# Kernel optimization log

Measured on AMD Instinct MI355X. Metric: run time of the kernel, lower is better.

Reference implementation:

```python
import jax, jax.numpy as jnp
import numpy as np

EPS = 1e-5


def setup_inputs() -> dict:
    key = jax.random.key(0)
    ks = jax.random.split(key, 8)
    g, p, d, h, w = 32, 64, 512, 24, 8
    hw = h * w
    return {
        "gal_fea": jax.random.normal(ks[0], (g, d, h, w), dtype=jnp.float32),
        "prob_fea": jax.random.normal(ks[1], (p, d, h, w), dtype=jnp.float32),
        "bn_weight": jnp.ones((1,), jnp.float32),
        "bn_bias": jnp.zeros((1,), jnp.float32),
        "bn_mean": jax.random.normal(ks[2], (1,), jnp.float32) * 0.1,
        "bn_var": jax.random.uniform(ks[3], (1,), jnp.float32, 0.5, 1.5),
        "fc_weight": jax.random.normal(ks[4], (1, 2 * hw), jnp.float32) * 0.05,
        "fc_bias": jnp.zeros((1,), jnp.float32),
        "lbn_weight": jnp.ones((1,), jnp.float32),
        "lbn_bias": jnp.zeros((1,), jnp.float32),
        "lbn_mean": jax.random.normal(ks[5], (1,), jnp.float32) * 0.1,
        "lbn_var": jax.random.uniform(ks[6], (1,), jnp.float32, 0.5, 1.5),
    }


def reference(gal_fea, prob_fea, bn_weight, bn_bias, bn_mean, bn_var,
              fc_weight, fc_bias, lbn_weight, lbn_bias, lbn_mean, lbn_var):
    g, d, h, w = gal_fea.shape
    p = prob_fea.shape[0]
    hw = h * w
    # 1x1 conv with probe pixels as kernels == batched correlation (QK^T style)
    gal = gal_fea.reshape(g, d, hw)                                  # [g, d, hw_x]
    ker = jnp.transpose(prob_fea, (0, 2, 3, 1)).reshape(p, hw, d)    # [p, hw_y, d]
    s = jnp.einsum('gdx,pyd->gpyx', gal, ker)                        # [g, p, hw_y, hw_x]
    # dual-axis max pooling, then concat: [g, p, 2*hw]
    score = jnp.concatenate([s.max(axis=2), s.max(axis=3)], axis=-1)
    # BatchNorm1d(1) in eval mode: scalar affine with running stats
    score = (score - bn_mean) * (bn_weight / jnp.sqrt(bn_var + EPS)) + bn_bias
    # fc: Linear(2*hw, 1)
    score = score.reshape(g * p, 2 * hw) @ fc_weight[0] + fc_bias[0]  # [g*p]
    score = score.reshape(g, p)
    # logit BatchNorm1d(1), eval mode
    score = (score - lbn_mean) * (lbn_weight / jnp.sqrt(lbn_var + EPS)) + lbn_bias
    return jax.nn.sigmoid(score / 10.0)
```

## Files before the change

### kernel.cpp

```cpp
#include <hip/hip_runtime.h>
#include <hip/hip_bf16.h>
#include <cstdint>
#include <cstddef>

#define NG 32
#define NP 64
#define ND 512
#define HW 192
#define KT2 16
#define EPSV 1e-5f

typedef _Float16 half8 __attribute__((ext_vector_type(8)));
typedef float floatx4 __attribute__((ext_vector_type(4)));
typedef float floatx16 __attribute__((ext_vector_type(16)));

__global__ __launch_bounds__(256) void prep_tiles(const float* __restrict__ gal,
                                                  const float* __restrict__ prob,
                                                  _Float16* __restrict__ galT3,
                                                  _Float16* __restrict__ probT3) {
  const int z = blockIdx.x;
  const int kt2 = blockIdx.y;
  const float* src;
  _Float16* dst;
  if (z < NP) {
    src = prob + (size_t)z * ND * HW;
    dst = probT3 + (size_t)z * KT2 * 6144;
  } else {
    src = gal + (size_t)(z - NP) * ND * HW;
    dst = galT3 + (size_t)(z - NP) * KT2 * 6144;
  }
  src += (size_t)kt2 * 32 * HW;
  dst += (size_t)kt2 * 6144;
  const int t = threadIdx.x;
#pragma unroll
  for (int r = 0; r < 3; ++r) {
    const int h = r * 256 + t;
    const int rb = h >> 7, kc = (h >> 6) & 1, hi = (h >> 5) & 1, l31 = h & 31;
    const float* sp = src + (size_t)(kc * 16 + hi * 8) * HW + rb * 32 + l31;
    half8 v;
#pragma unroll
    for (int j = 0; j < 8; ++j) v[j] = (_Float16)sp[(size_t)j * HW];
    *(half8*)(dst + (size_t)h * 8) = v;
  }
}

__device__ __forceinline__ void g2l16(const void* g, void* l) {
  __builtin_amdgcn_global_load_lds(
      (const __attribute__((address_space(1))) void*)g,
      (__attribute__((address_space(3))) void*)l, 16, 0, 0);
}

__global__ __launch_bounds__(256, 2) void qaconv_main(
    const _Float16* __restrict__ galT3, const _Float16* __restrict__ probT3,
    const float* __restrict__ bn_w, const float* __restrict__ bn_b,
    const float* __restrict__ bn_m, const float* __restrict__ bn_v,
    const float* __restrict__ fc_w, const float* __restrict__ fc_b,
    const float* __restrict__ lbn_w, const float* __restrict__ lbn_b,
    const float* __restrict__ lbn_m, const float* __restrict__ lbn_v,
    float* __restrict__ out) {
  __shared__ __align__(16) char shmem[50688];
  __shared__ float colp[2][HW];
  __shared__ float wsum[4];
  char* bufs = shmem;
  float(*rowbuf)[66] = (float(*)[66])shmem;

  const int bid = blockIdx.x;
  const int g = bid >> 6, p = bid & 63;

  const int t = threadIdx.x;
  const int lane = t & 63, wid = t >> 6;
  const int wr = wid & 1;
  const int wc = wid >> 1;
  const int l31 = lane & 31, hi = lane >> 5;

  const _Float16* pAl = probT3 + (size_t)p * KT2 * 6144 + wid * 512 + lane * 8;
  const _Float16* pBl = galT3 + (size_t)g * KT2 * 6144 + wid * 512 + lane * 8;
  const int sdst = wid * 1024;

  floatx16 acc[3][3];
#pragma unroll
  for (int ii = 0; ii < 3; ++ii)
#pragma unroll
    for (int jj = 0; jj < 3; ++jj) acc[ii][jj] = (floatx16)0.f;

#define STAGE(kt_, b_)                                               \
  {                                                                  \
    char* db_ = bufs + (b_)*24576 + sdst;                            \
    const _Float16* sa_ = pAl + (size_t)(kt_)*6144;                  \
    const _Float16* sb_ = pBl + (size_t)(kt_)*6144;                  \
    _Pragma("unroll") for (int r_ = 0; r_ < 3; ++r_)                 \
        g2l16(sa_ + (size_t)r_ * 2048, db_ + r_ * 4096);             \
    _Pragma("unroll") for (int r_ = 0; r_ < 3; ++r_)                 \
        g2l16(sb_ + (size_t)r_ * 2048, db_ + 12288 + r_ * 4096);     \
  }

#define KC_BODY(kc_)                                                             \
  {                                                                              \
    half8 af[3], bf[3];                                                          \
    const int off_ = (kc_)*1024 + hi * 512 + l31 * 16;                           \
    af[0] = *(const half8*)(bA + (wr * 3 + 0) * 2048 + off_);                    \
    af[1] = *(const half8*)(bA + (wr * 3 + 1) * 2048 + off_);                    \
    af[2] = *(const half8*)(bA + (wr * 3 + 2) * 2048 + off_);                    \
    bf[0] = *(const half8*)(bB + (wc * 3 + 0) * 2048 + off_);                    \
    bf[1] = *(const half8*)(bB + (wc * 3 + 1) * 2048 + off_);                    \
    bf[2] = *(const half8*)(bB + (wc * 3 + 2) * 2048 + off_);                    \
    __builtin_amdgcn_s_setprio(1);                                               \
    _Pragma("unroll") for (int ii = 0; ii < 3; ++ii)                             \
        _Pragma("unroll") for (int jj = 0; jj < 3; ++jj)                         \
            acc[ii][jj] = __builtin_amdgcn_mfma_f32_32x32x16_f16(af[ii], bf[jj], \
                                                                 acc[ii][jj], 0, 0, 0); \
    __builtin_amdgcn_s_setprio(0);                                               \
  }

  STAGE(0, 0);
  __syncthreads();

  for (int kt = 0; kt < KT2; ++kt) {
    if (kt < KT2 - 1) STAGE(kt + 1, (kt & 1) ^ 1);
    const char* bA = bufs + (kt & 1) * 24576;
    const char* bB = bA + 12288;
    KC_BODY(0)
    KC_BODY(1)
    __syncthreads();
  }

#pragma unroll
  for (int fb = 0; fb < 3; ++fb) {
    float v = -3.4e38f;
#pragma unroll
    for (int fa = 0; fa < 3; ++fa)
#pragma unroll
      for (int e = 0; e < 16; ++e) v = fmaxf(v, acc[fa][fb][e]);
    v = fmaxf(v, __shfl_xor(v, 32));
    if (lane < 32) colp[wr][wc * 96 + fb * 32 + lane] = v;
  }
#pragma unroll
  for (int fa = 0; fa < 3; ++fa)
#pragma unroll
    for (int e = 0; e < 16; ++e) {
      float rv = acc[fa][0][e];
      rv = fmaxf(rv, acc[fa][1][e]);
      rv = fmaxf(rv, acc[fa][2][e]);
      const int Y = wr * 96 + fa * 32 + (e & 3) + 8 * (e >> 2) + 4 * hi;
      rowbuf[Y][wc * 32 + l31] = rv;
    }
  __syncthreads();

  float partial = 0.f;
  if (t < HW) {
    const float* rb = rowbuf[t];
    float rmax = -3.4e38f;
#pragma unroll
    for (int j = 0; j < 16; ++j) {
      const floatx4 v = *(const floatx4*)&rb[j * 4];
      rmax = fmaxf(rmax, fmaxf(fmaxf(v[0], v[1]), fmaxf(v[2], v[3])));
    }
    const float cmax = fmaxf(colp[0][t], colp[1][t]);
    const float scale = bn_w[0] / sqrtf(bn_v[0] + EPSV);
    const float bm = bn_m[0], bb = bn_b[0];
    partial = ((cmax - bm) * scale + bb) * fc_w[t] +
              ((rmax - bm) * scale + bb) * fc_w[HW + t];
  }
#pragma unroll
  for (int off = 1; off < 64; off <<= 1) partial += __shfl_xor(partial, off);
  if (lane == 0) wsum[wid] = partial;
  __syncthreads();
  if (t == 0) {
    const float sum = fc_b[0] + wsum[0] + wsum[1] + wsum[2] + wsum[3];
    const float logit = (sum - lbn_m[0]) * (lbn_w[0] / sqrtf(lbn_v[0] + EPSV)) + lbn_b[0];
    out[bid] = 1.f / (1.f + expf(-logit * 0.1f));
  }
#undef STAGE
#undef KC_BODY
}

__global__ __launch_bounds__(256) void qaconv_naive(
    const float* __restrict__ gal, const float* __restrict__ prob,
    const float* __restrict__ bn_w, const float* __restrict__ bn_b,
    const float* __restrict__ bn_m, const float* __restrict__ bn_v,
    const float* __restrict__ fc_w, const float* __restrict__ fc_b,
    const float* __restrict__ lbn_w, const float* __restrict__ lbn_b,
    const float* __restrict__ lbn_m, const float* __restrict__ lbn_v,
    float* __restrict__ out) {
  __shared__ float prow[ND];
  __shared__ float rowmaxs[HW];
  __shared__ float colmaxs[HW];
  __shared__ float red[4];
  const int bid = blockIdx.x;
  const int g = bid >> 6, p = bid & 63;
  const int t = threadIdx.x, lane = t & 63, wid = t >> 6;
  const float* gp = gal + (size_t)g * ND * HW;
  const float* pp = prob + (size_t)p * ND * HW;
  float colmax = -3.4e38f;
  for (int y = 0; y < HW; ++y) {
    for (int k = t; k < ND; k += 256) prow[k] = pp[(size_t)k * HW + y];
    __syncthreads();
    float sv = -3.4e38f;
    if (t < HW) {
      sv = 0.f;
      for (int k = 0; k < ND; ++k) sv = fmaf(prow[k], gp[(size_t)k * HW + t], sv);
      colmax = fmaxf(colmax, sv);
    }
    float m = sv;
#pragma unroll
    for (int off = 1; off < 64; off <<= 1) m = fmaxf(m, __shfl_xor(m, off));
    if (lane == 0) red[wid] = m;
    __syncthreads();
    if (t == 0) rowmaxs[y] = fmaxf(fmaxf(red[0], red[1]), fmaxf(red[2], red[3]));
    __syncthreads();
  }
  if (t < HW) colmaxs[t] = colmax;
  __syncthreads();
  float partial = 0.f;
  for (int j = t; j < 2 * HW; j += 256) {
    const float v = (j < HW) ? colmaxs[j] : rowmaxs[j - HW];
    const float sc = (v - bn_m[0]) * (bn_w[0] / sqrtf(bn_v[0] + EPSV)) + bn_b[0];
    partial += sc * fc_w[j];
  }
#pragma unroll
  for (int off = 1; off < 64; off <<= 1) partial += __shfl_xor(partial, off);
  if (lane == 0) red[wid] = partial;
  __syncthreads();
  if (t == 0) {
    const float sum = fc_b[0] + red[0] + red[1] + red[2] + red[3];
    const float logit = (sum - lbn_m[0]) * (lbn_w[0] / sqrtf(lbn_v[0] + EPSV)) + lbn_b[0];
    out[bid] = 1.f / (1.f + expf(-logit * 0.1f));
  }
}

extern "C" void kernel_launch(void* const* d_in, const int* in_sizes, int n_in,
                              void* d_out, int out_size, void* d_ws, size_t ws_size,
                              hipStream_t stream) {
  const float* gal = (const float*)d_in[0];
  const float* prob = (const float*)d_in[1];
  const float* bn_w = (const float*)d_in[2];
  const float* bn_b = (const float*)d_in[3];
  const float* bn_m = (const float*)d_in[4];
  const float* bn_v = (const float*)d_in[5];
  const float* fc_w = (const float*)d_in[6];
  const float* fc_b = (const float*)d_in[7];
  const float* lbn_w = (const float*)d_in[8];
  const float* lbn_b = (const float*)d_in[9];
  const float* lbn_m = (const float*)d_in[10];
  const float* lbn_v = (const float*)d_in[11];
  float* out = (float*)d_out;

  const size_t probT3_elems = (size_t)NP * KT2 * 6144;
  const size_t galT3_elems = (size_t)NG * KT2 * 6144;
  const size_t ws_needed = (probT3_elems + galT3_elems) * sizeof(_Float16);
  if (ws_size >= ws_needed) {
    _Float16* probT3 = (_Float16*)d_ws;
    _Float16* galT3 = probT3 + probT3_elems;
    prep_tiles<<<dim3(NP + NG, KT2), dim3(256), 0, stream>>>(gal, prob, galT3, probT3);
    qaconv_main<<<dim3(NG * NP), dim3(256), 0, stream>>>(
        galT3, probT3, bn_w, bn_b, bn_m, bn_v, fc_w, fc_b, lbn_w, lbn_b, lbn_m, lbn_v, out);
  } else {
    qaconv_naive<<<dim3(NG * NP), dim3(256), 0, stream>>>(
        gal, prob, bn_w, bn_b, bn_m, bn_v, fc_w, fc_b, lbn_w, lbn_b, lbn_m, lbn_v, out);
  }
}
```

Before: 91.38 us.

## Load MFMA fragments directly from global memory, dropping LDS staging

The prep kernel now writes fp16 data in per-lane MFMA fragment order, with 16-deep k-slices staged through LDS so the reads from the source are coalesced. The main kernel loads its A/B fragments straight from global memory into registers, double-buffered in registers, and drops the LDS ping-pong buffers and the per-k-step barriers. The row-max reduction now uses cross-lane shuffles instead of a large LDS row buffer. This removes LDS traffic and synchronisation and frees shared memory. The cost is that every wave re-reads its fragments from global memory or L2, with more register pressure and less reuse across the waves in a block.

```diff
diff --git a/kernel.cpp b/kernel.cpp
--- a/kernel.cpp
+++ b/kernel.cpp
@@ -7,62 +7,59 @@
 #define NP 64
 #define ND 512
 #define HW 192
-#define KT2 16
+#define KS 32
 #define EPSV 1e-5f
 
 typedef _Float16 half8 __attribute__((ext_vector_type(8)));
 typedef float floatx4 __attribute__((ext_vector_type(4)));
 typedef float floatx16 __attribute__((ext_vector_type(16)));
 
-__global__ __launch_bounds__(256) void prep_tiles(const float* __restrict__ gal,
-                                                  const float* __restrict__ prob,
-                                                  _Float16* __restrict__ galT3,
-                                                  _Float16* __restrict__ probT3) {
+__global__ __launch_bounds__(256) void prep_frag(const float* __restrict__ gal,
+                                                 const float* __restrict__ prob,
+                                                 _Float16* __restrict__ galT4,
+                                                 _Float16* __restrict__ probT4) {
+  __shared__ float lds[16 * 192];
   const int z = blockIdx.x;
-  const int kt2 = blockIdx.y;
+  const int ks = blockIdx.y;
   const float* src;
   _Float16* dst;
   if (z < NP) {
     src = prob + (size_t)z * ND * HW;
-    dst = probT3 + (size_t)z * KT2 * 6144;
+    dst = probT4 + (size_t)z * 98304;
   } else {
     src = gal + (size_t)(z - NP) * ND * HW;
-    dst = galT3 + (size_t)(z - NP) * KT2 * 6144;
-  }
-  src += (size_t)kt2 * 32 * HW;
-  dst += (size_t)kt2 * 6144;
+    dst = galT4 + (size_t)(z - NP) * 98304;
+  }
+  src += (size_t)ks * 16 * HW;
+  dst += (size_t)ks * 3072;
   const int t = threadIdx.x;
 #pragma unroll
-  for (int r = 0; r < 3; ++r) {
+  for (int i = 0; i < 12; ++i) lds[i * 256 + t] = src[i * 256 + t];
+  __syncthreads();
+#pragma unroll
+  for (int r = 0; r < 2; ++r) {
     const int h = r * 256 + t;
-    const int rb = h >> 7, kc = (h >> 6) & 1, hi = (h >> 5) & 1, l31 = h & 31;
-    const float* sp = src + (size_t)(kc * 16 + hi * 8) * HW + rb * 32 + l31;
-    half8 v;
-#pragma unroll
-    for (int j = 0; j < 8; ++j) v[j] = (_Float16)sp[(size_t)j * HW];
-    *(half8*)(dst + (size_t)h * 8) = v;
-  }
-}
-
-__device__ __forceinline__ void g2l16(const void* g, void* l) {
-  __builtin_amdgcn_global_load_lds(
-      (const __attribute__((address_space(1))) void*)g,
-      (__attribute__((address_space(3))) void*)l, 16, 0, 0);
+    if (h < 384) {
+      const int rb = h >> 6, hi = (h >> 5) & 1, l31 = h & 31;
+      half8 v;
+#pragma unroll
+      for (int j = 0; j < 8; ++j) v[j] = (_Float16)lds[(hi * 8 + j) * 192 + rb * 32 + l31];
+      *(half8*)(dst + (size_t)h * 8) = v;
+    }
+  }
 }
 
 __global__ __launch_bounds__(256, 2) void qaconv_main(
-    const _Float16* __restrict__ galT3, const _Float16* __restrict__ probT3,
+    const _Float16* __restrict__ galT4, const _Float16* __restrict__ probT4,
     const float* __restrict__ bn_w, const float* __restrict__ bn_b,
     const float* __restrict__ bn_m, const float* __restrict__ bn_v,
     const float* __restrict__ fc_w, const float* __restrict__ fc_b,
     const float* __restrict__ lbn_w, const float* __restrict__ lbn_b,
     const float* __restrict__ lbn_m, const float* __restrict__ lbn_v,
     float* __restrict__ out) {
-  __shared__ __align__(16) char shmem[50688];
   __shared__ float colp[2][HW];
+  __shared__ float rowpart[2][HW];
   __shared__ float wsum[4];
-  char* bufs = shmem;
-  float(*rowbuf)[66] = (float(*)[66])shmem;
 
   const int bid = blockIdx.x;
   const int g = bid >> 6, p = bid & 63;
@@ -73,9 +70,8 @@
   const int wc = wid >> 1;
   const int l31 = lane & 31, hi = lane >> 5;
 
-  const _Float16* pAl = probT3 + (size_t)p * KT2 * 6144 + wid * 512 + lane * 8;
-  const _Float16* pBl = galT3 + (size_t)g * KT2 * 6144 + wid * 512 + lane * 8;
-  const int sdst = wid * 1024;
+  const _Float16* pA = probT4 + (size_t)p * 98304 + wr * 1536 + lane * 8;
+  const _Float16* pB = galT4 + (size_t)g * 98304 + wc * 1536 + lane * 8;
 
   floatx16 acc[3][3];
 #pragma unroll
@@ -83,45 +79,38 @@
 #pragma unroll
     for (int jj = 0; jj < 3; ++jj) acc[ii][jj] = (floatx16)0.f;
 
-#define STAGE(kt_, b_)                                               \
-  {                                                                  \
-    char* db_ = bufs + (b_)*24576 + sdst;                            \
-    const _Float16* sa_ = pAl + (size_t)(kt_)*6144;                  \
-    const _Float16* sb_ = pBl + (size_t)(kt_)*6144;                  \
-    _Pragma("unroll") for (int r_ = 0; r_ < 3; ++r_)                 \
-        g2l16(sa_ + (size_t)r_ * 2048, db_ + r_ * 4096);             \
-    _Pragma("unroll") for (int r_ = 0; r_ < 3; ++r_)                 \
-        g2l16(sb_ + (size_t)r_ * 2048, db_ + 12288 + r_ * 4096);     \
-  }
-
-#define KC_BODY(kc_)                                                             \
+#define LOADF(AF, BF, ks_)                                   \
+  {                                                          \
+    const _Float16* a_ = pA + (size_t)(ks_)*3072;            \
+    const _Float16* b_ = pB + (size_t)(ks_)*3072;            \
+    AF[0] = *(const half8*)(a_);                             \
+    AF[1] = *(const half8*)(a_ + 512);                       \
+    AF[2] = *(const half8*)(a_ + 1024);                      \
+    BF[0] = *(const half8*)(b_);                             \
+    BF[1] = *(const half8*)(b_ + 512);                       \
+    BF[2] = *(const half8*)(b_ + 1024);                      \
+  }
+
+#define MFMAS(AF, BF)                                                            \
   {                                                                              \
-    half8 af[3], bf[3];                                                          \
-    const int off_ = (kc_)*1024 + hi * 512 + l31 * 16;                           \
-    af[0] = *(const half8*)(bA + (wr * 3 + 0) * 2048 + off_);                    \
-    af[1] = *(const half8*)(bA + (wr * 3 + 1) * 2048 + off_);                    \
-    af[2] = *(const half8*)(bA + (wr * 3 + 2) * 2048 + off_);                    \
-    bf[0] = *(const half8*)(bB + (wc * 3 + 0) * 2048 + off_);                    \
-    bf[1] = *(const half8*)(bB + (wc * 3 + 1) * 2048 + off_);                    \
-    bf[2] = *(const half8*)(bB + (wc * 3 + 2) * 2048 + off_);                    \
     __builtin_amdgcn_s_setprio(1);                                               \
     _Pragma("unroll") for (int ii = 0; ii < 3; ++ii)                             \
         _Pragma("unroll") for (int jj = 0; jj < 3; ++jj)                         \
-            acc[ii][jj] = __builtin_amdgcn_mfma_f32_32x32x16_f16(af[ii], bf[jj], \
+            acc[ii][jj] = __builtin_amdgcn_mfma_f32_32x32x16_f16(AF[ii], BF[jj], \
                                                                  acc[ii][jj], 0, 0, 0); \
     __builtin_amdgcn_s_setprio(0);                                               \
   }
 
-  STAGE(0, 0);
-  __syncthreads();
-
-  for (int kt = 0; kt < KT2; ++kt) {
-    if (kt < KT2 - 1) STAGE(kt + 1, (kt & 1) ^ 1);
-    const char* bA = bufs + (kt & 1) * 24576;
-    const char* bB = bA + 12288;
-    KC_BODY(0)
-    KC_BODY(1)
-    __syncthreads();
+  half8 af0[3], bf0[3], af1[3], bf1[3];
+  LOADF(af0, bf0, 0)
+  LOADF(af1, bf1, 1)
+  for (int ks = 0; ks < KS; ks += 2) {
+    const int n0 = (ks + 2 < KS) ? ks + 2 : 30;
+    const int n1 = (ks + 3 < KS) ? ks + 3 : 31;
+    MFMAS(af0, bf0)
+    LOADF(af0, bf0, n0)
+    MFMAS(af1, bf1)
+    LOADF(af1, bf1, n1)
   }
 
 #pragma unroll
@@ -138,23 +127,22 @@
   for (int fa = 0; fa < 3; ++fa)
 #pragma unroll
     for (int e = 0; e < 16; ++e) {
-      float rv = acc[fa][0][e];
-      rv = fmaxf(rv, acc[fa][1][e]);
-      rv = fmaxf(rv, acc[fa][2][e]);
-      const int Y = wr * 96 + fa * 32 + (e & 3) + 8 * (e >> 2) + 4 * hi;
-      rowbuf[Y][wc * 32 + l31] = rv;
+      float rv = fmaxf(fmaxf(acc[fa][0][e], acc[fa][1][e]), acc[fa][2][e]);
+      rv = fmaxf(rv, __shfl_xor(rv, 1));
+      rv = fmaxf(rv, __shfl_xor(rv, 2));
+      rv = fmaxf(rv, __shfl_xor(rv, 4));
+      rv = fmaxf(rv, __shfl_xor(rv, 8));
+      rv = fmaxf(rv, __shfl_xor(rv, 16));
+      if (l31 == 0) {
+        const int Y = wr * 96 + fa * 32 + (e & 3) + 8 * (e >> 2) + 4 * hi;
+        rowpart[wc][Y] = rv;
+      }
     }
   __syncthreads();
 
   float partial = 0.f;
   if (t < HW) {
-    const float* rb = rowbuf[t];
-    float rmax = -3.4e38f;
-#pragma unroll
-    for (int j = 0; j < 16; ++j) {
-      const floatx4 v = *(const floatx4*)&rb[j * 4];
-      rmax = fmaxf(rmax, fmaxf(fmaxf(v[0], v[1]), fmaxf(v[2], v[3])));
-    }
+    const float rmax = fmaxf(rowpart[0][t], rowpart[1][t]);
     const float cmax = fmaxf(colp[0][t], colp[1][t]);
     const float scale = bn_w[0] / sqrtf(bn_v[0] + EPSV);
     const float bm = bn_m[0], bb = bn_b[0];
@@ -170,8 +158,8 @@
     const float logit = (sum - lbn_m[0]) * (lbn_w[0] / sqrtf(lbn_v[0] + EPSV)) + lbn_b[0];
     out[bid] = 1.f / (1.f + expf(-logit * 0.1f));
   }
-#undef STAGE
-#undef KC_BODY
+#undef LOADF
+#undef MFMAS
 }
 
 __global__ __launch_bounds__(256) void qaconv_naive(
@@ -245,15 +233,15 @@
   const float* lbn_v = (const float*)d_in[11];
   float* out = (float*)d_out;
 
-  const size_t probT3_elems = (size_t)NP * KT2 * 6144;
-  const size_t galT3_elems = (size_t)NG * KT2 * 6144;
-  const size_t ws_needed = (probT3_elems + galT3_elems) * sizeof(_Float16);
+  const size_t probT4_elems = (size_t)NP * 98304;
+  const size_t galT4_elems = (size_t)NG * 98304;
+  const size_t ws_needed = (probT4_elems + galT4_elems) * sizeof(_Float16);
   if (ws_size >= ws_needed) {
-    _Float16* probT3 = (_Float16*)d_ws;
-    _Float16* galT3 = probT3 + probT3_elems;
-    prep_tiles<<<dim3(NP + NG, KT2), dim3(256), 0, stream>>>(gal, prob, galT3, probT3);
+    _Float16* probT4 = (_Float16*)d_ws;
+    _Float16* galT4 = probT4 + probT4_elems;
+    prep_frag<<<dim3(NP + NG, KS), dim3(256), 0, stream>>>(gal, prob, galT4, probT4);
     qaconv_main<<<dim3(NG * NP), dim3(256), 0, stream>>>(
-        galT3, probT3, bn_w, bn_b, bn_m, bn_v, fc_w, fc_b, lbn_w, lbn_b, lbn_m, lbn_v, out);
+        galT4, probT4, bn_w, bn_b, bn_m, bn_v, fc_w, fc_b, lbn_w, lbn_b, lbn_m, lbn_v, out);
   } else {
     qaconv_naive<<<dim3(NG * NP), dim3(256), 0, stream>>>(
         gal, prob, bn_w, bn_b, bn_m, bn_v, fc_w, fc_b, lbn_w, lbn_b, lbn_m, lbn_v, out);
```

New measurement: 109.2 us. 19.5% more time.
